# Performance work log

Hardware: AMD Instinct MI355X
Metric: run time of the kernel (lower is better)

The kernel has to match this reference:

```python
import jax, jax.numpy as jnp
import numpy as np

N_HEADS = 16
N_KV_HEADS = 4
HEAD_DIM = 64
ROPE_BASE = 10000.0

def _rope_cos_sin(T, dtype):
    # flash-attn style: cos/sin of shape [T, head_dim//2]
    inv_freq = 1.0 / (ROPE_BASE ** (jnp.arange(0, HEAD_DIM, 2, dtype=jnp.float32) / HEAD_DIM))
    freqs = jnp.arange(T, dtype=jnp.float32)[:, None] * inv_freq[None, :]  # [T, D/2]
    return jnp.cos(freqs).astype(dtype), jnp.sin(freqs).astype(dtype)

def _apply_rope(x, cos, sin):
    # x: [B, H, T, D], non-interleaved rotate-half on full head dim
    d2 = HEAD_DIM // 2
    x1, x2 = x[..., :d2], x[..., d2:]
    c = cos[None, None, :, :]
    s = sin[None, None, :, :]
    return jnp.concatenate([x1 * c - x2 * s, x2 * c + x1 * s], axis=-1)

def setup_inputs() -> dict:
    key = jax.random.key(0)
    ks = jax.random.split(key, 6)
    B, T, D = 1, 4096, 1024
    def g(k, shape, scale):
        return jax.random.normal(k, shape, dtype=jnp.float32) * scale
    return {
        "query": g(ks[0], (B, T, D), 1.0),
        "Wq": g(ks[1], (D, D), D ** -0.5),
        "Wk": g(ks[2], (D, N_KV_HEADS * HEAD_DIM), D ** -0.5),
        "Wv": g(ks[3], (D, N_KV_HEADS * HEAD_DIM), D ** -0.5),
        "W1": g(ks[4], (D, 4 * D), D ** -0.5),
        "W2": g(ks[5], (4 * D, D), (4 * D) ** -0.5),
    }

def reference(query, Wq, Wk, Wv, W1, W2):
    B, T, D = query.shape
    # QKV projections -> [B, H, T, Dh]
    q = (query @ Wq).reshape(B, T, N_HEADS, HEAD_DIM).transpose(0, 2, 1, 3)
    k = (query @ Wk).reshape(B, T, N_KV_HEADS, HEAD_DIM).transpose(0, 2, 1, 3)
    v = (query @ Wv).reshape(B, T, N_KV_HEADS, HEAD_DIM).transpose(0, 2, 1, 3)
    # RoPE (seqlen_offset = 0, no cache)
    cos, sin = _rope_cos_sin(T, q.dtype)
    q = _apply_rope(q, cos, sin)
    k = _apply_rope(k, cos, sin)
    # GQA: repeat KV heads to match Q heads
    n_rep = N_HEADS // N_KV_HEADS
    k = jnp.repeat(k, n_rep, axis=1)
    v = jnp.repeat(v, n_rep, axis=1)
    # Scaled dot-product attention, causal
    scale = HEAD_DIM ** -0.5
    scores = jnp.einsum("bhqd,bhkd->bhqk", q, k) * scale
    i = jnp.arange(T)[:, None]
    j = jnp.arange(T)[None, :]
    scores = jnp.where(j > i, jnp.finfo(scores.dtype).min, scores)
    attn = jax.nn.softmax(scores, axis=-1)
    out = jnp.einsum("bhqk,bhkd->bhqd", attn, v)  # [B, H, T, Dh]
    out = out.transpose(0, 2, 1, 3).reshape(B, T, D)
    # out_proj: Linear -> SiLU -> Linear (use_swiglu=True path)
    return jax.nn.silu(out @ W1) @ W2
```

## Files before the change

### kernel.cpp

```cpp
#include <hip/hip_runtime.h>
#include <stdint.h>

typedef unsigned short u16;
typedef __bf16 bf16x8 __attribute__((ext_vector_type(8)));
typedef float f32x4 __attribute__((ext_vector_type(4)));

#define T_SEQ 4096
#define DMODEL 1024

__device__ __forceinline__ float bf2f(u16 x) {
  union { uint32_t u; float f; } v; v.u = ((uint32_t)x) << 16; return v.f;
}
__device__ __forceinline__ u16 f2bf(float f) {
  union { float f; uint32_t u; } v; v.f = f;
  return (u16)((v.u + 0x7FFFu + ((v.u >> 16) & 1u)) >> 16);
}
__device__ __forceinline__ float fexp2(float x) {
#if __has_builtin(__builtin_amdgcn_exp2f)
  return __builtin_amdgcn_exp2f(x);
#else
  return __expf(x * 0.6931471805599453f);
#endif
}
__device__ __forceinline__ uint32_t pack_bf16(float lo, float hi) {
#if __has_builtin(__builtin_amdgcn_cvt_pk_bf16_f32)
  typedef __bf16 bf16x2_t __attribute__((ext_vector_type(2)));
  union { bf16x2_t v; uint32_t u; } c;
  c.v = __builtin_amdgcn_cvt_pk_bf16_f32(lo, hi);
  return c.u;
#else
  union { float f; uint32_t u; } a, b;
  a.f = lo; b.f = hi;
  return __builtin_amdgcn_perm(b.u + 0x8000u, a.u + 0x8000u, 0x07060302u);
#endif
}
__device__ __forceinline__ void async16(void* lds, const void* g) {
  __builtin_amdgcn_global_load_lds(
      (__attribute__((address_space(1))) void*)const_cast<void*>(g),
      (__attribute__((address_space(3))) void*)lds, 16, 0, 0);
}
__device__ __forceinline__ void storeC(u16* C, size_t i, float v) { C[i] = f2bf(v); }
__device__ __forceinline__ void storeC(float* C, size_t i, float v) { C[i] = v; }

__device__ __forceinline__ void wtrans_body(const float* __restrict__ in,
                                            u16* __restrict__ out, int K, int N,
                                            int bx, int by, int tid,
                                            float (*tile)[65]) {
  const int n0 = bx * 64, k0 = by * 64;
  const int r = tid >> 2, c = (tid & 3) * 16;
#pragma unroll
  for (int j = 0; j < 4; ++j) {
    float4 v = *(const float4*)&in[(size_t)(k0 + r) * N + n0 + c + j * 4];
    tile[r][c + j * 4 + 0] = v.x; tile[r][c + j * 4 + 1] = v.y;
    tile[r][c + j * 4 + 2] = v.z; tile[r][c + j * 4 + 3] = v.w;
  }
  __syncthreads();
  union { u16 s[16]; uint4 q[2]; } buf;
#pragma unroll
  for (int j = 0; j < 16; ++j) buf.s[j] = f2bf(tile[c + j][r]);
  u16* dst = out + (size_t)(n0 + r) * K + k0 + c;
  *(uint4*)(dst) = buf.q[0];
  *(uint4*)(dst + 8) = buf.q[1];
}

__global__ void __launch_bounds__(256) prep(const float* __restrict__ query,
                                            const float* __restrict__ Wq,
                                            const float* __restrict__ Wk,
                                            const float* __restrict__ Wv,
                                            const float* __restrict__ W1,
                                            const float* __restrict__ W2,
                                            u16* __restrict__ Xb,
                                            u16* __restrict__ WqkvT,
                                            u16* __restrict__ W1T,
                                            u16* __restrict__ W2T) {
  __shared__ float tile[64][65];
  const int b = blockIdx.x, tid = threadIdx.x;
  if (b < 4096) {
    int idx = (b * 256 + tid) * 4;
    float4 v = *(const float4*)(query + idx);
    union { u16 s[4]; uint2 q; } o;
    o.s[0] = f2bf(v.x); o.s[1] = f2bf(v.y); o.s[2] = f2bf(v.z); o.s[3] = f2bf(v.w);
    *(uint2*)(Xb + idx) = o.q;
  } else if (b < 4352) {
    int t = b - 4096;
    wtrans_body(Wq, WqkvT, 1024, 1024, t & 15, t >> 4, tid, tile);
  } else if (b < 4416) {
    int t = b - 4352;
    wtrans_body(Wk, WqkvT + (size_t)1024 * 1024, 1024, 256, t & 3, t >> 2, tid, tile);
  } else if (b < 4480) {
    int t = b - 4416;
    wtrans_body(Wv, WqkvT + (size_t)1280 * 1024, 1024, 256, t & 3, t >> 2, tid, tile);
  } else if (b < 5504) {
    int t = b - 4480;
    wtrans_body(W1, W1T, 1024, 4096, t & 63, t >> 6, tid, tile);
  } else {
    int t = b - 5504;
    wtrans_body(W2, W2T, 4096, 1024, t & 15, t >> 4, tid, tile);
  }
}

__global__ void __launch_bounds__(256) rope_vt(const u16* __restrict__ qkv,
                                               u16* __restrict__ Q,
                                               u16* __restrict__ Ko,
                                               u16* __restrict__ Vt) {
  __shared__ u16 tile[64][65];
  const int b = blockIdx.x, tid = threadIdx.x;
  if (b < 4096) {
    const int t = b;
    const int i = tid & 31;
    const float ang = (float)t * powf(10000.f, -(float)i * (1.f / 32.f));
    float s, c;
    sincosf(ang, &s, &c);
    const u16* row = qkv + (size_t)t * 1536;
    const float QS = 0.125f * 1.4426950408889634f;
    const float cq = c * QS, sq = s * QS;
#pragma unroll
    for (int it = 0; it < 2; ++it) {
      int h = (tid >> 5) + it * 8;
      float x1 = bf2f(row[h * 64 + i]);
      float x2 = bf2f(row[h * 64 + 32 + i]);
      size_t o = ((size_t)h * T_SEQ + t) * 64 + i;
      Q[o] = f2bf(x1 * cq - x2 * sq);
      Q[o + 32] = f2bf(x2 * cq + x1 * sq);
    }
    if (tid < 128) {
      int h = tid >> 5;
      float x1 = bf2f(row[1024 + h * 64 + i]);
      float x2 = bf2f(row[1024 + h * 64 + 32 + i]);
      size_t o = ((size_t)h * T_SEQ + t) * 64 + i;
      Ko[o] = f2bf(x1 * c - x2 * s);
      Ko[o + 32] = f2bf(x2 * c + x1 * s);
    }
  } else {
    const int t = b - 4096;
    const int t0 = (t & 63) * 64, h = t >> 6;
    const int r = tid >> 2, q4 = (tid & 3) * 16;
    const u16* src = qkv + (size_t)(t0 + r) * 1536 + 1280 + h * 64 + q4;
    union { u16 s[16]; uint4 q[2]; } buf;
    buf.q[0] = *(const uint4*)(src);
    buf.q[1] = *(const uint4*)(src + 8);
#pragma unroll
    for (int j = 0; j < 16; ++j) tile[r][q4 + j] = buf.s[j];
    __syncthreads();
#pragma unroll
    for (int j = 0; j < 16; ++j) buf.s[j] = tile[q4 + j][r];
    u16* dst = Vt + ((size_t)h * 64 + r) * T_SEQ + t0 + q4;
    *(uint4*)(dst) = buf.q[0];
    *(uint4*)(dst + 8) = buf.q[1];
  }
}

template <int AM, int ACT, typename OutT>
__global__ void __launch_bounds__(256) gemm_bt(const u16* __restrict__ A,
                                               const u16* __restrict__ Bt,
                                               OutT* __restrict__ C,
                                               int M, int N, int K) {
  __shared__ u16 sA[2][AM * 32][64];
  __shared__ u16 sB[2][128][64];
  const int tid = threadIdx.x;
  const int w = tid >> 6, lane = tid & 63;
  const int g = lane >> 4, l15 = lane & 15;
  const int r8 = lane >> 3, c8 = lane & 7;
  const int bm = blockIdx.y * (AM * 32), bn = blockIdx.x * 128;

  f32x4 acc[AM][4];
#pragma unroll
  for (int i = 0; i < AM; ++i)
#pragma unroll
    for (int j = 0; j < 4; ++j) acc[i][j] = (f32x4){0.f, 0.f, 0.f, 0.f};

  const u16* Ag = A + (size_t)(bm + w * (AM * 8) + r8) * K + (c8 ^ r8) * 8;
  const u16* Bg = Bt + (size_t)(bn + w * 32 + r8) * K + (c8 ^ r8) * 8;
  const int mrow = (w >> 1) * (AM * 16), ncol = (w & 1) * 64;
  const int swz = l15 & 7;

#define GSTAGE(K0, BUF)                                                        \
  {                                                                            \
    _Pragma("unroll") for (int t = 0; t < AM; ++t)                             \
      async16(&sA[BUF][w * (AM * 8) + t * 8][0], Ag + (size_t)(t * 8) * K + (K0)); \
    _Pragma("unroll") for (int t = 0; t < 4; ++t)                              \
      async16(&sB[BUF][w * 32 + t * 8][0], Bg + (size_t)(t * 8) * K + (K0));   \
  }

  GSTAGE(0, 0);
  int cur = 0;
  for (int k0 = 0; k0 < K; k0 += 64) {
    __syncthreads();
    if (k0 + 64 < K) GSTAGE(k0 + 64, cur ^ 1);
#pragma unroll
    for (int kk = 0; kk < 2; ++kk) {
      const int cb = ((kk * 4 + g) ^ swz) * 8;
      bf16x8 a[AM], b[4];
#pragma unroll
      for (int i = 0; i < AM; ++i) a[i] = *(const bf16x8*)&sA[cur][mrow + i * 16 + l15][cb];
#pragma unroll
      for (int i = 0; i < 4; ++i) b[i] = *(const bf16x8*)&sB[cur][ncol + i * 16 + l15][cb];
#pragma unroll
      for (int mi = 0; mi < AM; ++mi)
#pragma unroll
        for (int ni = 0; ni < 4; ++ni)
          acc[mi][ni] = __builtin_amdgcn_mfma_f32_16x16x32_bf16(a[mi], b[ni], acc[mi][ni], 0, 0, 0);
    }
    cur ^= 1;
  }
#undef GSTAGE
#pragma unroll
  for (int mi = 0; mi < AM; ++mi)
#pragma unroll
    for (int ni = 0; ni < 4; ++ni)
#pragma unroll
      for (int r = 0; r < 4; ++r) {
        int row = bm + mrow + mi * 16 + g * 4 + r;
        int col = bn + ncol + ni * 16 + l15;
        float v = acc[mi][ni][r];
        if (ACT == 1) v = v / (1.f + __expf(-v));
        storeC(C, (size_t)row * N + col, v);
      }
}

__global__ void __launch_bounds__(256, 2) gemm_w2(const u16* __restrict__ A,
                                                  const u16* __restrict__ Bt,
                                                  float* __restrict__ C0,
                                                  u16* __restrict__ C1) {
  __shared__ u16 sA[2][128][64];
  __shared__ u16 sB[2][128][64];
  const int K = 4096, N = 1024;
  const int z = blockIdx.z, koff = z * 2048;
  const int tid = threadIdx.x;
  const int w = tid >> 6, lane = tid & 63;
  const int g = lane >> 4, l15 = lane & 15;
  const int r8 = lane >> 3, c8 = lane & 7;
  const int bm = blockIdx.y * 128, bn = blockIdx.x * 128;

  f32x4 acc[4][4];
#pragma unroll
  for (int i = 0; i < 4; ++i)
#pragma unroll
    for (int j = 0; j < 4; ++j) acc[i][j] = (f32x4){0.f, 0.f, 0.f, 0.f};

  const u16* Ag = A + (size_t)(bm + w * 32 + r8) * K + koff + (c8 ^ r8) * 8;
  const u16* Bg = Bt + (size_t)(bn + w * 32 + r8) * K + koff + (c8 ^ r8) * 8;
  const int mrow = (w >> 1) * 64, ncol = (w & 1) * 64;
  const int swz = l15 & 7;

#define GSTAGE(K0, BUF)                                                   \
  {                                                                       \
    _Pragma("unroll") for (int t = 0; t < 4; ++t) {                       \
      async16(&sA[BUF][w * 32 + t * 8][0], Ag + (size_t)(t * 8) * K + (K0)); \
      async16(&sB[BUF][w * 32 + t * 8][0], Bg + (size_t)(t * 8) * K + (K0)); \
    }                                                                     \
  }

  GSTAGE(0, 0);
  int cur = 0;
  for (int k0 = 0; k0 < 2048; k0 += 64) {
    __syncthreads();
    if (k0 + 64 < 2048) GSTAGE(k0 + 64, cur ^ 1);
#pragma unroll
    for (int kk = 0; kk < 2; ++kk) {
      const int cb = ((kk * 4 + g) ^ swz) * 8;
      bf16x8 a[4], b[4];
#pragma unroll
      for (int i = 0; i < 4; ++i) {
        a[i] = *(const bf16x8*)&sA[cur][mrow + i * 16 + l15][cb];
        b[i] = *(const bf16x8*)&sB[cur][ncol + i * 16 + l15][cb];
      }
#pragma unroll
      for (int mi = 0; mi < 4; ++mi)
#pragma unroll
        for (int ni = 0; ni < 4; ++ni)
          acc[mi][ni] = __builtin_amdgcn_mfma_f32_16x16x32_bf16(a[mi], b[ni], acc[mi][ni], 0, 0, 0);
    }
    cur ^= 1;
  }
#undef GSTAGE
#pragma unroll
  for (int mi = 0; mi < 4; ++mi)
#pragma unroll
    for (int ni = 0; ni < 4; ++ni)
#pragma unroll
      for (int r = 0; r < 4; ++r) {
        size_t idx = (size_t)(bm + mrow + mi * 16 + g * 4 + r) * N + bn + ncol + ni * 16 + l15;
        if (z == 0) C0[idx] = acc[mi][ni][r];
        else        C1[idx] = f2bf(acc[mi][ni][r]);
      }
}

__global__ void __launch_bounds__(256) w2_combine(float* __restrict__ out,
                                                  const u16* __restrict__ P1) {
  int idx = (blockIdx.x * 256 + threadIdx.x) * 4;
  float4 v = *(const float4*)(out + idx);
  union { uint2 q; u16 s[4]; } p;
  p.q = *(const uint2*)(P1 + idx);
  v.x += bf2f(p.s[0]); v.y += bf2f(p.s[1]);
  v.z += bf2f(p.s[2]); v.w += bf2f(p.s[3]);
  *(float4*)(out + idx) = v;
}

__global__ void __launch_bounds__(256, 2) attn(const u16* __restrict__ Q,
                                               const u16* __restrict__ K,
                                               const u16* __restrict__ Vt,
                                               u16* __restrict__ O0,
                                               u16* __restrict__ O1,
                                               float* __restrict__ L0,
                                               float* __restrict__ L1) {
  __shared__ u16 sK[2][64][64];
  __shared__ u16 sV[2][64][64];
  __shared__ u16 sP[4][64][68];
  const int pr = blockIdx.x >> 1;
  const int split = blockIdx.x & 1;
  const int h = blockIdx.y;
  const int kvh = h >> 2;
  const int tid = threadIdx.x;
  const int w = tid >> 6, lane = tid & 63;
  const int g = lane >> 4, l15 = lane & 15;
  const int r8 = lane >> 3, c8 = lane & 7;
  const int swz = l15 & 7;
  const int t0 = pr, t1 = 31 - pr;
  const int off = split * 64;

  u16* Op = split ? O1 : O0;
  float* Lp = split ? L1 : L0;

  bf16x8 qf[2][2][2];
  {
    const u16* Qh = Q + (size_t)h * T_SEQ * 64;
#pragma unroll
    for (int half = 0; half < 2; ++half)
#pragma unroll
      for (int mi = 0; mi < 2; ++mi) {
        const int q = (half ? t1 : t0) * 128 + w * 32 + mi * 16 + l15;
#pragma unroll
        for (int kk = 0; kk < 2; ++kk)
          qf[half][mi][kk] = *(const bf16x8*)(Qh + (size_t)q * 64 + (kk * 4 + g) * 8);
      }
  }

  f32x4 oacc[2][2][4];
  f32x4 lacc[2][2];
#pragma unroll
  for (int half = 0; half < 2; ++half)
#pragma unroll
    for (int mi = 0; mi < 2; ++mi) {
      lacc[half][mi] = (f32x4){0.f, 0.f, 0.f, 0.f};
#pragma unroll
      for (int nd = 0; nd < 4; ++nd) oacc[half][mi][nd] = (f32x4){0.f, 0.f, 0.f, 0.f};
    }

  bf16x8 ONES;
  {
    union { u16 s[8]; bf16x8 v; } o;
#pragma unroll
    for (int i = 0; i < 8; ++i) o.s[i] = 0x3F80;
    ONES = o.v;
  }

  const u16* Kg = K + ((size_t)kvh * T_SEQ + w * 16 + r8) * 64 + (c8 ^ r8) * 8;
  const u16* Vg = Vt + ((size_t)kvh * 64 + w * 16 + r8) * T_SEQ + (c8 ^ r8) * 8;

#define STAGE(J, B)                                                     \
  {                                                                     \
    const int kv0_ = (J) * 64;                                          \
    async16(&sK[B][w * 16 + 0][0], Kg + (size_t)kv0_ * 64);             \
    async16(&sK[B][w * 16 + 8][0], Kg + (size_t)(kv0_ + 8) * 64);       \
    async16(&sV[B][w * 16 + 0][0], Vg + kv0_);                          \
    async16(&sV[B][w * 16 + 8][0], Vg + (size_t)8 * T_SEQ + kv0_);      \
  }

#define BODY(B, ACT0, M0, M1)                                                     \
  {                                                                               \
    const int b_ = (B);                                                           \
    f32x4 s1[2][4], s0[2][4];                                                     \
    _Pragma("unroll") for (int mi = 0; mi < 2; ++mi)                              \
    _Pragma("unroll") for (int kt = 0; kt < 4; ++kt) {                            \
      s1[mi][kt] = (f32x4){0.f, 0.f, 0.f, 0.f};                                   \
      if (ACT0) s0[mi][kt] = (f32x4){0.f, 0.f, 0.f, 0.f};                         \
    }                                                                             \
    __builtin_amdgcn_s_setprio(1);                                                \
    _Pragma("unroll") for (int kt = 0; kt < 4; ++kt)                              \
    _Pragma("unroll") for (int kk = 0; kk < 2; ++kk) {                            \
      bf16x8 kf = *(const bf16x8*)&sK[b_][kt * 16 + l15][((kk * 4 + g) ^ swz) * 8]; \
      _Pragma("unroll") for (int mi = 0; mi < 2; ++mi) {                          \
        s1[mi][kt] = __builtin_amdgcn_mfma_f32_16x16x32_bf16(kf, qf[1][mi][kk], s1[mi][kt], 0, 0, 0); \
        if (ACT0)                                                                 \
          s0[mi][kt] = __builtin_amdgcn_mfma_f32_16x16x32_bf16(kf, qf[0][mi][kk], s0[mi][kt], 0, 0, 0); \
      }                                                                           \
    }                                                                             \
    __builtin_amdgcn_s_setprio(0);                                                \
    _Pragma("unroll") for (int mi = 0; mi < 2; ++mi) {                            \
      const int thr_ = w * 32 + mi * 16 + l15 - off;                              \
      _Pragma("unroll") for (int kt = 0; kt < 4; ++kt) {                          \
        float p_[4];                                                              \
        _Pragma("unroll") for (int r = 0; r < 4; ++r) {                           \
          float p = fexp2(s1[mi][kt][r]);                                         \
          if (M1 && (kt * 16 + g * 4 + r > thr_)) p = 0.f;                        \
          p_[r] = p;                                                              \
        }                                                                         \
        uint2 pk;                                                                 \
        pk.x = pack_bf16(p_[0], p_[1]);                                           \
        pk.y = pack_bf16(p_[2], p_[3]);                                           \
        *(uint2*)&sP[w][32 + mi * 16 + l15][kt * 16 + g * 4] = pk;                \
      }                                                                           \
      if (ACT0) {                                                                 \
        _Pragma("unroll") for (int kt = 0; kt < 4; ++kt) {                        \
          float p_[4];                                                            \
          _Pragma("unroll") for (int r = 0; r < 4; ++r) {                         \
            float p = fexp2(s0[mi][kt][r]);                                       \
            if (M0 && (kt * 16 + g * 4 + r > thr_)) p = 0.f;                      \
            p_[r] = p;                                                            \
          }                                                                       \
          uint2 pk;                                                               \
          pk.x = pack_bf16(p_[0], p_[1]);                                         \
          pk.y = pack_bf16(p_[2], p_[3]);                                         \
          *(uint2*)&sP[w][mi * 16 + l15][kt * 16 + g * 4] = pk;                   \
        }                                                                         \
      }                                                                           \
    }                                                                             \
    __builtin_amdgcn_wave_barrier();          \
    __builtin_amdgcn_s_setprio(1);                                                \
    _Pragma("unroll") for (int kk = 0; kk < 2; ++kk) {                            \
      bf16x8 pf1[2], pf0[2];                                                      \
      _Pragma("unroll") for (int mi = 0; mi < 2; ++mi) {                          \
        pf1[mi] = *(const bf16x8*)&sP[w][32 + mi * 16 + l15][kk * 32 + g * 8];    \
        if (ACT0) pf0[mi] = *(const bf16x8*)&sP[w][mi * 16 + l15][kk * 32 + g * 8]; \
      }                                                                           \
      _Pragma("unroll") for (int mi = 0; mi < 2; ++mi) {                          \
        lacc[1][mi] = __builtin_amdgcn_mfma_f32_16x16x32_bf16(pf1[mi], ONES, lacc[1][mi], 0, 0, 0); \
        if (ACT0)                                                                 \
          lacc[0][mi] = __builtin_amdgcn_mfma_f32_16x16x32_bf16(pf0[mi], ONES, lacc[0][mi], 0, 0, 0); \
      }                                                                           \
      _Pragma("unroll") for (int nd = 0; nd < 4; ++nd) {                          \
        bf16x8 vf = *(const bf16x8*)&sV[b_][nd * 16 + l15][((kk * 4 + g) ^ swz) * 8]; \
        _Pragma("unroll") for (int mi = 0; mi < 2; ++mi) {                        \
          oacc[1][mi][nd] = __builtin_amdgcn_mfma_f32_16x16x32_bf16(pf1[mi], vf, oacc[1][mi][nd], 0, 0, 0); \
          if (ACT0)                                                               \
            oacc[0][mi][nd] = __builtin_amdgcn_mfma_f32_16x16x32_bf16(pf0[mi], vf, oacc[0][mi][nd], 0, 0, 0); \
        }                                                                         \
      }                                                                           \
    }                                                                             \
    __builtin_amdgcn_s_setprio(0);                                                \
  }

  const int e0 = 2 * t0 + split, e1 = 2 * t1 + split;
  STAGE(split, 0);
  int jj = split, b = 0;
  for (; jj < e0; jj += 2, b ^= 1) {
    __syncthreads();
    STAGE(jj + 2, b ^ 1);
    BODY(b, true, false, false);
  }
  {
    __syncthreads();
    STAGE(jj + 2, b ^ 1);
    BODY(b, true, true, false);
    jj += 2; b ^= 1;
  }
  for (; jj < e1; jj += 2, b ^= 1) {
    __syncthreads();
    STAGE(jj + 2, b ^ 1);
    BODY(b, false, false, false);
  }
  {
    __syncthreads();
    BODY(b, false, false, true);
  }
#undef STAGE
#undef BODY

#pragma unroll
  for (int half = 0; half < 2; ++half) {
    const int tb = (half ? t1 : t0) * 128;
#pragma unroll
    for (int mi = 0; mi < 2; ++mi)
#pragma unroll
      for (int r = 0; r < 4; ++r) {
        const int trow = tb + w * 32 + mi * 16 + g * 4 + r;
#pragma unroll
        for (int nd = 0; nd < 4; ++nd)
          Op[(size_t)trow * DMODEL + h * 64 + nd * 16 + l15] = f2bf(oacc[half][mi][nd][r]);
        if (l15 == 0) Lp[h * T_SEQ + trow] = lacc[half][mi][r];
      }
  }
}

__global__ void __launch_bounds__(256) attn_combine(const u16* __restrict__ O0,
                                                    const u16* __restrict__ O1,
                                                    const float* __restrict__ L0,
                                                    const float* __restrict__ L1,
                                                    u16* __restrict__ AO) {
  const int t = blockIdx.x, tid = threadIdx.x;
  const int h = tid >> 4, d4 = (tid & 15) * 4;
  const float inv = 1.f / (L0[h * T_SEQ + t] + L1[h * T_SEQ + t]);
  const size_t idx = (size_t)t * DMODEL + h * 64 + d4;
  union { uint2 q; u16 s[4]; } a, b, o;
  a.q = *(const uint2*)(O0 + idx);
  b.q = *(const uint2*)(O1 + idx);
#pragma unroll
  for (int i = 0; i < 4; ++i) o.s[i] = f2bf((bf2f(a.s[i]) + bf2f(b.s[i])) * inv);
  *(uint2*)(AO + idx) = o.q;
}

extern "C" void kernel_launch(void* const* d_in, const int* in_sizes, int n_in,
                              void* d_out, int out_size, void* d_ws, size_t ws_size,
                              hipStream_t stream) {
  const float* query = (const float*)d_in[0];
  const float* Wq = (const float*)d_in[1];
  const float* Wk = (const float*)d_in[2];
  const float* Wv = (const float*)d_in[3];
  const float* W1 = (const float*)d_in[4];
  const float* W2 = (const float*)d_in[5];
  float* out = (float*)d_out;

  char* ws = (char*)d_ws;
  size_t off = 0;
  auto alloc = [&](size_t bytes) { char* p = ws + off; off += (bytes + 255) & ~(size_t)255; return p; };
  u16* Xb   = (u16*)alloc((size_t)4096 * 1024 * 2);
  u16* QKVb = (u16*)alloc((size_t)4096 * 1536 * 2);
  u16* Qb   = (u16*)alloc((size_t)16 * 4096 * 64 * 2);
  u16* Kb   = (u16*)alloc((size_t)4 * 4096 * 64 * 2);
  u16* Vtb  = (u16*)alloc((size_t)4 * 4096 * 64 * 2);
  u16* H    = (u16*)ws;
  u16*   O0p = Xb;
  u16*   O1p = QKVb;
  float* L0p = (float*)(QKVb + (size_t)4096 * 1024);
  float* L1p = L0p + 16 * T_SEQ;
  u16* WqkvT = (u16*)alloc((size_t)1536 * 1024 * 2);
  u16* W1T   = (u16*)alloc((size_t)4096 * 1024 * 2);
  u16* W2T   = (u16*)alloc((size_t)1024 * 4096 * 2);
  u16* AO    = (u16*)alloc((size_t)4096 * 1024 * 2);
  u16* P1    = W1T;
  (void)ws_size; (void)in_sizes; (void)n_in; (void)out_size;

  prep<<<6528, 256, 0, stream>>>(query, Wq, Wk, Wv, W1, W2, Xb, WqkvT, W1T, W2T);
  gemm_bt<2, 0, u16><<<dim3(12, 64), 256, 0, stream>>>(Xb, WqkvT, QKVb, 4096, 1536, 1024);
  rope_vt<<<4352, 256, 0, stream>>>(QKVb, Qb, Kb, Vtb);
  attn<<<dim3(32, 16), 256, 0, stream>>>(Qb, Kb, Vtb, O0p, O1p, L0p, L1p);
  attn_combine<<<4096, 256, 0, stream>>>(O0p, O1p, L0p, L1p, AO);
  gemm_bt<4, 1, u16><<<dim3(32, 32), 256, 0, stream>>>(AO, W1T, H, 4096, 4096, 1024);
  gemm_w2<<<dim3(8, 32, 2), 256, 0, stream>>>(H, W2T, out, P1);
  w2_combine<<<4096, 256, 0, stream>>>(out, P1);
}
```

Before: 278.4 us.

## Software-pipeline attention loop so PV of previous tile overlaps QK of next

```diff
diff --git a/kernel.cpp b/kernel.cpp
--- a/kernel.cpp
+++ b/kernel.cpp
@@ -305,7 +305,7 @@
                                                float* __restrict__ L0,
                                                float* __restrict__ L1) {
   __shared__ u16 sK[2][64][64];
-  __shared__ u16 sV[2][64][64];
+  __shared__ u16 sV[3][64][64];
   __shared__ u16 sP[4][64][68];
   const int pr = blockIdx.x >> 1;
   const int split = blockIdx.x & 1;
@@ -358,19 +358,20 @@
   const u16* Kg = K + ((size_t)kvh * T_SEQ + w * 16 + r8) * 64 + (c8 ^ r8) * 8;
   const u16* Vg = Vt + ((size_t)kvh * 64 + w * 16 + r8) * T_SEQ + (c8 ^ r8) * 8;
 
-#define STAGE(J, B)                                                     \
+  f32x4 s1[2][4], s0[2][4];
+  uint2 pk1[2][4], pk0[2][4];
+
+#define STAGE2(J, KB, VB)                                               \
   {                                                                     \
     const int kv0_ = (J) * 64;                                          \
-    async16(&sK[B][w * 16 + 0][0], Kg + (size_t)kv0_ * 64);             \
-    async16(&sK[B][w * 16 + 8][0], Kg + (size_t)(kv0_ + 8) * 64);       \
-    async16(&sV[B][w * 16 + 0][0], Vg + kv0_);                          \
-    async16(&sV[B][w * 16 + 8][0], Vg + (size_t)8 * T_SEQ + kv0_);      \
-  }
-
-#define BODY(B, ACT0, M0, M1)                                                     \
+    async16(&sK[KB][w * 16 + 0][0], Kg + (size_t)kv0_ * 64);            \
+    async16(&sK[KB][w * 16 + 8][0], Kg + (size_t)(kv0_ + 8) * 64);      \
+    async16(&sV[VB][w * 16 + 0][0], Vg + kv0_);                         \
+    async16(&sV[VB][w * 16 + 8][0], Vg + (size_t)8 * T_SEQ + kv0_);     \
+  }
+
+#define QKMM(B, ACT0)                                                             \
   {                                                                               \
-    const int b_ = (B);                                                           \
-    f32x4 s1[2][4], s0[2][4];                                                     \
     _Pragma("unroll") for (int mi = 0; mi < 2; ++mi)                              \
     _Pragma("unroll") for (int kt = 0; kt < 4; ++kt) {                            \
       s1[mi][kt] = (f32x4){0.f, 0.f, 0.f, 0.f};                                   \
@@ -379,7 +380,7 @@
     __builtin_amdgcn_s_setprio(1);                                                \
     _Pragma("unroll") for (int kt = 0; kt < 4; ++kt)                              \
     _Pragma("unroll") for (int kk = 0; kk < 2; ++kk) {                            \
-      bf16x8 kf = *(const bf16x8*)&sK[b_][kt * 16 + l15][((kk * 4 + g) ^ swz) * 8]; \
+      bf16x8 kf = *(const bf16x8*)&sK[B][kt * 16 + l15][((kk * 4 + g) ^ swz) * 8]; \
       _Pragma("unroll") for (int mi = 0; mi < 2; ++mi) {                          \
         s1[mi][kt] = __builtin_amdgcn_mfma_f32_16x16x32_bf16(kf, qf[1][mi][kk], s1[mi][kt], 0, 0, 0); \
         if (ACT0)                                                                 \
@@ -387,6 +388,36 @@
       }                                                                           \
     }                                                                             \
     __builtin_amdgcn_s_setprio(0);                                                \
+  }
+
+#define PVL(PACT0, VB)                                                            \
+  {                                                                               \
+    __builtin_amdgcn_s_setprio(1);                                                \
+    _Pragma("unroll") for (int kk = 0; kk < 2; ++kk) {                            \
+      bf16x8 pf1[2], pf0[2];                                                      \
+      _Pragma("unroll") for (int mi = 0; mi < 2; ++mi) {                          \
+        pf1[mi] = *(const bf16x8*)&sP[w][32 + mi * 16 + l15][kk * 32 + g * 8];    \
+        if (PACT0) pf0[mi] = *(const bf16x8*)&sP[w][mi * 16 + l15][kk * 32 + g * 8]; \
+      }                                                                           \
+      _Pragma("unroll") for (int mi = 0; mi < 2; ++mi) {                          \
+        lacc[1][mi] = __builtin_amdgcn_mfma_f32_16x16x32_bf16(pf1[mi], ONES, lacc[1][mi], 0, 0, 0); \
+        if (PACT0)                                                                \
+          lacc[0][mi] = __builtin_amdgcn_mfma_f32_16x16x32_bf16(pf0[mi], ONES, lacc[0][mi], 0, 0, 0); \
+      }                                                                           \
+      _Pragma("unroll") for (int nd = 0; nd < 4; ++nd) {                          \
+        bf16x8 vf = *(const bf16x8*)&sV[VB][nd * 16 + l15][((kk * 4 + g) ^ swz) * 8]; \
+        _Pragma("unroll") for (int mi = 0; mi < 2; ++mi) {                        \
+          oacc[1][mi][nd] = __builtin_amdgcn_mfma_f32_16x16x32_bf16(pf1[mi], vf, oacc[1][mi][nd], 0, 0, 0); \
+          if (PACT0)                                                              \
+            oacc[0][mi][nd] = __builtin_amdgcn_mfma_f32_16x16x32_bf16(pf0[mi], vf, oacc[0][mi][nd], 0, 0, 0); \
+        }                                                                         \
+      }                                                                           \
+    }                                                                             \
+    __builtin_amdgcn_s_setprio(0);                                                \
+  }
+
+#define EXPPK(ACT0, M0, M1)                                                       \
+  {                                                                               \
     _Pragma("unroll") for (int mi = 0; mi < 2; ++mi) {                            \
       const int thr_ = w * 32 + mi * 16 + l15 - off;                              \
       _Pragma("unroll") for (int kt = 0; kt < 4; ++kt) {                          \
@@ -396,76 +427,105 @@
           if (M1 && (kt * 16 + g * 4 + r > thr_)) p = 0.f;                        \
           p_[r] = p;                                                              \
         }                                                                         \
-        uint2 pk;                                                                 \
-        pk.x = pack_bf16(p_[0], p_[1]);                                           \
-        pk.y = pack_bf16(p_[2], p_[3]);                                           \
-        *(uint2*)&sP[w][32 + mi * 16 + l15][kt * 16 + g * 4] = pk;                \
-      }                                                                           \
-      if (ACT0) {                                                                 \
-        _Pragma("unroll") for (int kt = 0; kt < 4; ++kt) {                        \
-          float p_[4];                                                            \
+        pk1[mi][kt].x = pack_bf16(p_[0], p_[1]);                                  \
+        pk1[mi][kt].y = pack_bf16(p_[2], p_[3]);                                  \
+        if (ACT0) {                                                               \
+          float q_[4];                                                            \
           _Pragma("unroll") for (int r = 0; r < 4; ++r) {                         \
             float p = fexp2(s0[mi][kt][r]);                                       \
             if (M0 && (kt * 16 + g * 4 + r > thr_)) p = 0.f;                      \
-            p_[r] = p;                                                            \
+            q_[r] = p;                                                            \
           }                                                                       \
-          uint2 pk;                                                               \
-          pk.x = pack_bf16(p_[0], p_[1]);                                         \
-          pk.y = pack_bf16(p_[2], p_[3]);                                         \
-          *(uint2*)&sP[w][mi * 16 + l15][kt * 16 + g * 4] = pk;                   \
+          pk0[mi][kt].x = pack_bf16(q_[0], q_[1]);                                \
+          pk0[mi][kt].y = pack_bf16(q_[2], q_[3]);                                \
         }                                                                         \
       }                                                                           \
     }                                                                             \
-    __builtin_amdgcn_wave_barrier();          \
-    __builtin_amdgcn_s_setprio(1);                                                \
-    _Pragma("unroll") for (int kk = 0; kk < 2; ++kk) {                            \
-      bf16x8 pf1[2], pf0[2];                                                      \
-      _Pragma("unroll") for (int mi = 0; mi < 2; ++mi) {                          \
-        pf1[mi] = *(const bf16x8*)&sP[w][32 + mi * 16 + l15][kk * 32 + g * 8];    \
-        if (ACT0) pf0[mi] = *(const bf16x8*)&sP[w][mi * 16 + l15][kk * 32 + g * 8]; \
-      }                                                                           \
-      _Pragma("unroll") for (int mi = 0; mi < 2; ++mi) {                          \
-        lacc[1][mi] = __builtin_amdgcn_mfma_f32_16x16x32_bf16(pf1[mi], ONES, lacc[1][mi], 0, 0, 0); \
-        if (ACT0)                                                                 \
-          lacc[0][mi] = __builtin_amdgcn_mfma_f32_16x16x32_bf16(pf0[mi], ONES, lacc[0][mi], 0, 0, 0); \
-      }                                                                           \
-      _Pragma("unroll") for (int nd = 0; nd < 4; ++nd) {                          \
-        bf16x8 vf = *(const bf16x8*)&sV[b_][nd * 16 + l15][((kk * 4 + g) ^ swz) * 8]; \
-        _Pragma("unroll") for (int mi = 0; mi < 2; ++mi) {                        \
-          oacc[1][mi][nd] = __builtin_amdgcn_mfma_f32_16x16x32_bf16(pf1[mi], vf, oacc[1][mi][nd], 0, 0, 0); \
-          if (ACT0)                                                               \
-            oacc[0][mi][nd] = __builtin_amdgcn_mfma_f32_16x16x32_bf16(pf0[mi], vf, oacc[0][mi][nd], 0, 0, 0); \
-        }                                                                         \
-      }                                                                           \
+  }
+
+#define SPW(ACT0)                                                                 \
+  {                                                                               \
+    _Pragma("unroll") for (int mi = 0; mi < 2; ++mi)                              \
+    _Pragma("unroll") for (int kt = 0; kt < 4; ++kt) {                            \
+      *(uint2*)&sP[w][32 + mi * 16 + l15][kt * 16 + g * 4] = pk1[mi][kt];         \
+      if (ACT0) *(uint2*)&sP[w][mi * 16 + l15][kt * 16 + g * 4] = pk0[mi][kt];    \
     }                                                                             \
-    __builtin_amdgcn_s_setprio(0);                                                \
-  }
-
-  const int e0 = 2 * t0 + split, e1 = 2 * t1 + split;
-  STAGE(split, 0);
-  int jj = split, b = 0;
-  for (; jj < e0; jj += 2, b ^= 1) {
-    __syncthreads();
-    STAGE(jj + 2, b ^ 1);
-    BODY(b, true, false, false);
-  }
-  {
-    __syncthreads();
-    STAGE(jj + 2, b ^ 1);
-    BODY(b, true, true, false);
-    jj += 2; b ^= 1;
-  }
-  for (; jj < e1; jj += 2, b ^= 1) {
-    __syncthreads();
-    STAGE(jj + 2, b ^ 1);
-    BODY(b, false, false, false);
-  }
-  {
-    __syncthreads();
-    BODY(b, false, false, true);
-  }
-#undef STAGE
-#undef BODY
+  }
+
+  STAGE2(split, 0, 0);
+  __syncthreads();
+  STAGE2(split + 2, 1, 1);
+  QKMM(0, true);
+  if (t0 == 0) { EXPPK(true, true, false); }
+  else         { EXPPK(true, false, false); }
+  SPW(true);
+  int b = 1;
+  int vp = 0, vc = 1, vn = 2;
+  int i = 1;
+  for (; i < t0; ++i) {
+    __syncthreads();
+    STAGE2(split + 2 * (i + 1), b ^ 1, vn);
+    QKMM(b, true);
+    PVL(true, vp);
+    EXPPK(true, false, false);
+    __builtin_amdgcn_wave_barrier();
+    SPW(true);
+    b ^= 1; int tmp = vp; vp = vc; vc = vn; vn = tmp;
+  }
+  if (t0 >= 1) {
+    __syncthreads();
+    STAGE2(split + 2 * (i + 1), b ^ 1, vn);
+    QKMM(b, true);
+    PVL(true, vp);
+    EXPPK(true, true, false);
+    __builtin_amdgcn_wave_barrier();
+    SPW(true);
+    b ^= 1; int tmp = vp; vp = vc; vc = vn; vn = tmp;
+    ++i;
+  }
+  if (i < t1) {
+    __syncthreads();
+    STAGE2(split + 2 * (i + 1), b ^ 1, vn);
+    QKMM(b, false);
+    PVL(true, vp);
+    EXPPK(false, false, false);
+    __builtin_amdgcn_wave_barrier();
+    SPW(false);
+    b ^= 1; { int tmp = vp; vp = vc; vc = vn; vn = tmp; }
+    ++i;
+    for (; i < t1; ++i) {
+      __syncthreads();
+      STAGE2(split + 2 * (i + 1), b ^ 1, vn);
+      QKMM(b, false);
+      PVL(false, vp);
+      EXPPK(false, false, false);
+      __builtin_amdgcn_wave_barrier();
+      SPW(false);
+      b ^= 1; int tmp = vp; vp = vc; vc = vn; vn = tmp;
+    }
+    __syncthreads();
+    QKMM(b, false);
+    PVL(false, vp);
+    EXPPK(false, false, true);
+    __builtin_amdgcn_wave_barrier();
+    SPW(false);
+    __builtin_amdgcn_wave_barrier();
+    PVL(false, vc);
+  } else {
+    __syncthreads();
+    QKMM(b, false);
+    PVL(true, vp);
+    EXPPK(false, false, true);
+    __builtin_amdgcn_wave_barrier();
+    SPW(false);
+    __builtin_amdgcn_wave_barrier();
+    PVL(false, vc);
+  }
+#undef STAGE2
+#undef QKMM
+#undef PVL
+#undef EXPPK
+#undef SPW
 
 #pragma unroll
   for (int half = 0; half < 2; ++half) {
```

New measurement: 283.7 us. About the same (+1.9%).

## Enlarge FFN GEMM tiles to 256-wide with 512-thread blocks

Applied to the files above, without the earlier changes.

```diff
diff --git a/kernel.cpp b/kernel.cpp
--- a/kernel.cpp
+++ b/kernel.cpp
@@ -218,11 +218,79 @@
       }
 }
 
-__global__ void __launch_bounds__(256, 2) gemm_w2(const u16* __restrict__ A,
+__global__ void __launch_bounds__(512, 2) gemm_ffn1(const u16* __restrict__ A,
+                                                    const u16* __restrict__ Bt,
+                                                    u16* __restrict__ C) {
+  const int N = 4096, K = 1024;
+  __shared__ u16 sA[2][256][64];
+  __shared__ u16 sB[2][256][64];
+  const int tid = threadIdx.x;
+  const int w = tid >> 6, lane = tid & 63;
+  const int g = lane >> 4, l15 = lane & 15;
+  const int r8 = lane >> 3, c8 = lane & 7;
+  const int wm = w >> 2, wn = w & 3;
+  const int bm = blockIdx.y * 256, bn = blockIdx.x * 256;
+
+  f32x4 acc[8][4];
+#pragma unroll
+  for (int i = 0; i < 8; ++i)
+#pragma unroll
+    for (int j = 0; j < 4; ++j) acc[i][j] = (f32x4){0.f, 0.f, 0.f, 0.f};
+
+  const u16* Ag = A + (size_t)(bm + w * 32 + r8) * K + (c8 ^ r8) * 8;
+  const u16* Bg = Bt + (size_t)(bn + w * 32 + r8) * K + (c8 ^ r8) * 8;
+  const int mrow = wm * 128, ncol = wn * 64;
+  const int swz = l15 & 7;
+
+#define FSTAGE(K0, BUF)                                                   \
+  {                                                                       \
+    _Pragma("unroll") for (int t = 0; t < 4; ++t) {                       \
+      async16(&sA[BUF][w * 32 + t * 8][0], Ag + (size_t)(t * 8) * K + (K0)); \
+      async16(&sB[BUF][w * 32 + t * 8][0], Bg + (size_t)(t * 8) * K + (K0)); \
+    }                                                                     \
+  }
+
+  FSTAGE(0, 0);
+  int cur = 0;
+  for (int k0 = 0; k0 < K; k0 += 64) {
+    __syncthreads();
+    if (k0 + 64 < K) FSTAGE(k0 + 64, cur ^ 1);
+#pragma unroll
+    for (int kk = 0; kk < 2; ++kk) {
+      const int cb = ((kk * 4 + g) ^ swz) * 8;
+      bf16x8 a[8], b[4];
+#pragma unroll
+      for (int i = 0; i < 8; ++i) a[i] = *(const bf16x8*)&sA[cur][mrow + i * 16 + l15][cb];
+#pragma unroll
+      for (int i = 0; i < 4; ++i) b[i] = *(const bf16x8*)&sB[cur][ncol + i * 16 + l15][cb];
+#pragma unroll
+      for (int mi = 0; mi < 8; ++mi)
+#pragma unroll
+        for (int ni = 0; ni < 4; ++ni)
+          acc[mi][ni] = __builtin_amdgcn_mfma_f32_16x16x32_bf16(a[mi], b[ni], acc[mi][ni], 0, 0, 0);
+    }
+    cur ^= 1;
+  }
+#undef FSTAGE
+#pragma unroll
+  for (int mi = 0; mi < 8; ++mi)
+#pragma unroll
+    for (int ni = 0; ni < 4; ++ni)
+#pragma unroll
+      for (int r = 0; r < 4; ++r) {
+        int row = bm + mrow + mi * 16 + g * 4 + r;
+        int col = bn + ncol + ni * 16 + l15;
+        float v = acc[mi][ni][r];
+        v = v / (1.f + __expf(-v));
+        C[(size_t)row * N + col] = f2bf(v);
+      }
+}
+
+__global__ void __launch_bounds__(512, 2) gemm_w2(const u16* __restrict__ A,
                                                   const u16* __restrict__ Bt,
                                                   float* __restrict__ C0,
                                                   u16* __restrict__ C1) {
-  __shared__ u16 sA[2][128][64];
+  __shared__ u16 sA[2][256][64];
   __shared__ u16 sB[2][128][64];
   const int K = 4096, N = 1024;
   const int z = blockIdx.z, koff = z * 2048;
@@ -230,7 +298,8 @@
   const int w = tid >> 6, lane = tid & 63;
   const int g = lane >> 4, l15 = lane & 15;
   const int r8 = lane >> 3, c8 = lane & 7;
-  const int bm = blockIdx.y * 128, bn = blockIdx.x * 128;
+  const int wm = w >> 1, wn = w & 1;
+  const int bm = blockIdx.y * 256, bn = blockIdx.x * 128;
 
   f32x4 acc[4][4];
 #pragma unroll
@@ -239,16 +308,16 @@
     for (int j = 0; j < 4; ++j) acc[i][j] = (f32x4){0.f, 0.f, 0.f, 0.f};
 
   const u16* Ag = A + (size_t)(bm + w * 32 + r8) * K + koff + (c8 ^ r8) * 8;
-  const u16* Bg = Bt + (size_t)(bn + w * 32 + r8) * K + koff + (c8 ^ r8) * 8;
-  const int mrow = (w >> 1) * 64, ncol = (w & 1) * 64;
+  const u16* Bg = Bt + (size_t)(bn + w * 16 + r8) * K + koff + (c8 ^ r8) * 8;
+  const int mrow = wm * 64, ncol = wn * 64;
   const int swz = l15 & 7;
 
 #define GSTAGE(K0, BUF)                                                   \
   {                                                                       \
-    _Pragma("unroll") for (int t = 0; t < 4; ++t) {                       \
+    _Pragma("unroll") for (int t = 0; t < 4; ++t)                         \
       async16(&sA[BUF][w * 32 + t * 8][0], Ag + (size_t)(t * 8) * K + (K0)); \
-      async16(&sB[BUF][w * 32 + t * 8][0], Bg + (size_t)(t * 8) * K + (K0)); \
-    }                                                                     \
+    _Pragma("unroll") for (int t = 0; t < 2; ++t)                         \
+      async16(&sB[BUF][w * 16 + t * 8][0], Bg + (size_t)(t * 8) * K + (K0)); \
   }
 
   GSTAGE(0, 0);
@@ -536,7 +605,7 @@
   rope_vt<<<4352, 256, 0, stream>>>(QKVb, Qb, Kb, Vtb);
   attn<<<dim3(32, 16), 256, 0, stream>>>(Qb, Kb, Vtb, O0p, O1p, L0p, L1p);
   attn_combine<<<4096, 256, 0, stream>>>(O0p, O1p, L0p, L1p, AO);
-  gemm_bt<4, 1, u16><<<dim3(32, 32), 256, 0, stream>>>(AO, W1T, H, 4096, 4096, 1024);
-  gemm_w2<<<dim3(8, 32, 2), 256, 0, stream>>>(H, W2T, out, P1);
+  gemm_ffn1<<<dim3(16, 16), 512, 0, stream>>>(AO, W1T, H);
+  gemm_w2<<<dim3(8, 16, 2), 512, 0, stream>>>(H, W2T, out, P1);
   w2_combine<<<4096, 256, 0, stream>>>(out, P1);
 }
```

Measured after the change: 284.1 us. 1.02x slower.
